# Kernel optimization log

Measured on AMD Instinct MI355X. Metric: run time of the kernel, lower is better.

The kernel has to match this reference:

```python
import jax, jax.numpy as jnp
import numpy as np

B, N, C = 8, 1024, 1024
H = 16
D = C // H  # head_dim = 64
SCALE = D ** -0.5


def setup_inputs() -> dict:
    key = jax.random.key(0)
    k1, k2, k3, k4 = jax.random.split(key, 4)
    x = jax.random.normal(k1, (B, N, C), dtype=jnp.float32)
    qkv_w = jax.random.normal(k2, (3 * C, C), dtype=jnp.float32) * (C ** -0.5)
    proj_w = jax.random.normal(k3, (C, C), dtype=jnp.float32) * (C ** -0.5)
    proj_b = jax.random.normal(k4, (C,), dtype=jnp.float32)
    return {"x": x, "qkv_w": qkv_w, "proj_w": proj_w, "proj_b": proj_b}


def reference(x, qkv_w, proj_w, proj_b):
    # qkv projection: torch Linear weight is [out, in] -> x @ W^T
    qkv = jnp.einsum('bnc,oc->bno', x, qkv_w)            # [B, N, 3C]
    qkv = qkv.reshape(B, N, 3, H, D)
    q = jnp.transpose(qkv[:, :, 0], (0, 2, 1, 3))        # [B, H, N, D]
    k = jnp.transpose(qkv[:, :, 1], (0, 2, 1, 3))
    v = jnp.transpose(qkv[:, :, 2], (0, 2, 1, 3))
    attn = jnp.einsum('bhqd,bhkd->bhqk', q, k) * SCALE   # [B, H, N, N]
    attn = jax.nn.softmax(attn, axis=-1)
    out = jnp.einsum('bhqk,bhkd->bhqd', attn, v)         # [B, H, N, D]
    out = jnp.transpose(out, (0, 2, 1, 3)).reshape(B, N, C)
    out = jnp.einsum('bnc,oc->bno', out, proj_w) + proj_b
    return out
```

## Files before the change

kernel.cpp:

```cpp
#include <hip/hip_runtime.h>
#include <hip/hip_bf16.h>
#include <stdint.h>

#define B_ 8
#define N_ 1024
#define C_ 1024
#define H_ 16

static constexpr float SCALE = 0.125f;
static constexpr float LOG2E = 1.4426950408889634f;
static constexpr float SL    = SCALE * LOG2E;

typedef __attribute__((ext_vector_type(4))) float f32x4;
typedef __attribute__((ext_vector_type(8))) short s16x8;

__device__ __forceinline__ ushort f2bf(float f) {
    union { float f; uint32_t u; } c; c.f = f;
    uint32_t u = c.u;
    return (ushort)((u + 0x7fffu + ((u >> 16) & 1u)) >> 16);
}

__device__ __forceinline__ ushort f2bfc(float f) {
    union { __hip_bfloat16 h; ushort u; } c;
    c.h = __float2bfloat16(f);
    return c.u;
}

__device__ __forceinline__ void gload_lds16(const void* g, void* l) {
    __builtin_amdgcn_global_load_lds(
        (const __attribute__((address_space(1))) void*)g,
        (__attribute__((address_space(3))) void*)l,
        16, 0, 0);
}
__device__ __forceinline__ void gload_lds4(const void* g, void* l) {
    __builtin_amdgcn_global_load_lds(
        (const __attribute__((address_space(1))) void*)g,
        (__attribute__((address_space(3))) void*)l,
        4, 0, 0);
}

__global__ __launch_bounds__(256) void cvt_all(const float* __restrict__ x,
                                               const float* __restrict__ qkv_w,
                                               const float* __restrict__ proj_w,
                                               ushort* __restrict__ xb,
                                               ushort* __restrict__ wqkv,
                                               ushort* __restrict__ wproj) {
    int i = blockIdx.x * 256 + threadIdx.x;
    const float* src;
    ushort* dst;
    float sc = 1.0f;
    if (i < 2097152) {
        src = x; dst = xb;
    } else if (i < 2097152 + 786432) {
        i -= 2097152;
        src = qkv_w; dst = wqkv;
        if (i < 262144) sc = SL;
    } else {
        i -= 2097152 + 786432;
        src = proj_w; dst = wproj;
    }
    float4 v = ((const float4*)src)[i];
    ushort4 o = make_ushort4(f2bf(v.x * sc), f2bf(v.y * sc), f2bf(v.z * sc), f2bf(v.w * sc));
    ((ushort4*)dst)[i] = o;
}

template<int OUT_BF16>
__global__ __launch_bounds__(256) void gemm_bt(const ushort* __restrict__ A,
                                               const ushort* __restrict__ Bw,
                                               void* __restrict__ Cout,
                                               const float* __restrict__ bias,
                                               int M, int Nout, int K) {
    __shared__ ushort Asm[128 * 64];
    __shared__ ushort Bsm[128 * 64];
    const int t = threadIdx.x;
    const int l = t & 63, w = t >> 6;
    const int lq = l & 15, lg = l >> 4;
    const int trow = blockIdx.y * 128, tcol = blockIdx.x * 128;
    const int wrow = (w >> 1) * 64, wcol = (w & 1) * 64;

    f32x4 acc[4][4] = {};

    const int srow0 = t >> 3;
    const int sc8 = (((t & 7) ^ (srow0 & 7)) * 8);
    const size_t abase = (size_t)(trow + srow0) * K + sc8;
    const size_t bbase = (size_t)(tcol + srow0) * K + sc8;

    for (int k0 = 0; k0 < K; k0 += 64) {
#pragma unroll
        for (int i = 0; i < 4; ++i) {
            gload_lds16(A + abase + (size_t)i * 32 * K + k0, &Asm[(i * 256 + w * 64) * 8]);
            gload_lds16(Bw + bbase + (size_t)i * 32 * K + k0, &Bsm[(i * 256 + w * 64) * 8]);
        }
        __syncthreads();
#pragma unroll
        for (int kk = 0; kk < 2; ++kk) {
            s16x8 af[4], bf[4];
#pragma unroll
            for (int m = 0; m < 4; ++m) {
                int row = wrow + m * 16 + lq;
                int ch = (kk * 4 + lg) ^ (row & 7);
                af[m] = *(const s16x8*)&Asm[row * 64 + ch * 8];
            }
#pragma unroll
            for (int n = 0; n < 4; ++n) {
                int row = wcol + n * 16 + lq;
                int ch = (kk * 4 + lg) ^ (row & 7);
                bf[n] = *(const s16x8*)&Bsm[row * 64 + ch * 8];
            }
#pragma unroll
            for (int m = 0; m < 4; ++m)
#pragma unroll
                for (int n = 0; n < 4; ++n)
                    acc[m][n] = __builtin_amdgcn_mfma_f32_16x16x32_bf16(af[m], bf[n], acc[m][n], 0, 0, 0);
        }
        __syncthreads();
    }

#pragma unroll
    for (int m = 0; m < 4; ++m)
#pragma unroll
        for (int n = 0; n < 4; ++n)
#pragma unroll
            for (int r = 0; r < 4; ++r) {
                int row = trow + wrow + m * 16 + lg * 4 + r;
                int col = tcol + wcol + n * 16 + lq;
                if (OUT_BF16) {
                    ((ushort*)Cout)[(size_t)row * Nout + col] = f2bfc(acc[m][n][r]);
                } else {
                    ((float*)Cout)[(size_t)row * Nout + col] = acc[m][n][r] + bias[col];
                }
            }
}

__global__ __launch_bounds__(512, 2) void gemm_bt256(const ushort* __restrict__ A,
                                                     const ushort* __restrict__ Bw,
                                                     ushort* __restrict__ Cout,
                                                     int M, int Nout, int K) {
    __shared__ ushort Asm[2][256 * 64];
    __shared__ ushort Bsm[2][256 * 64];
    const int t = threadIdx.x;
    const int l = t & 63, w = t >> 6;
    const int lq = l & 15, lg = l >> 4;
    const int wm = w >> 2, wn = w & 3;

    int bid = blockIdx.y * gridDim.x + blockIdx.x;
    const int cpx = (gridDim.x * gridDim.y) >> 3;
    bid = (bid & 7) * cpx + (bid >> 3);
    const int bx = bid % gridDim.x, by = bid / gridDim.x;
    const int trow = by * 256, tcol = bx * 256;

    f32x4 acc[8][4] = {};

    const int srow = t >> 3;
    const int scc = ((t & 7) ^ (srow & 7)) * 8;
    const size_t abase = (size_t)(trow + srow) * K + scc;
    const size_t bbase = (size_t)(tcol + srow) * K + scc;

#define STAGE256(buf, k0)                                                      \
    {                                                                          \
        _Pragma("unroll")                                                      \
        for (int j = 0; j < 4; ++j) {                                          \
            gload_lds16(A + abase + (size_t)j * 64 * K + (k0),                 \
                        &Asm[buf][(j * 512 + t) * 8]);                         \
            gload_lds16(Bw + bbase + (size_t)j * 64 * K + (k0),                \
                        &Bsm[buf][(j * 512 + t) * 8]);                         \
        }                                                                      \
    }
#define LOAD_A256(qr)                                                          \
    _Pragma("unroll") for (int m = 0; m < 4; ++m) {                            \
        const int row = wm * 128 + (qr) * 64 + m * 16 + lq;                    \
        _Pragma("unroll") for (int kk = 0; kk < 2; ++kk)                       \
            af[m][kk] = *(const s16x8*)&Asm[cur][row * 64 +                    \
                            (((kk * 4 + lg) ^ (row & 7)) * 8)];                \
    }
#define LOAD_B256(qc)                                                          \
    _Pragma("unroll") for (int n = 0; n < 2; ++n) {                            \
        const int row = wn * 64 + (qc) * 32 + n * 16 + lq;                     \
        _Pragma("unroll") for (int kk = 0; kk < 2; ++kk)                       \
            bf[n][kk] = *(const s16x8*)&Bsm[cur][row * 64 +                    \
                            (((kk * 4 + lg) ^ (row & 7)) * 8)];                \
    }
#define MFMA_Q256(qr, qc)                                                      \
    __builtin_amdgcn_s_setprio(1);                                             \
    _Pragma("unroll") for (int m = 0; m < 4; ++m)                              \
        _Pragma("unroll") for (int n = 0; n < 2; ++n)                          \
            _Pragma("unroll") for (int kk = 0; kk < 2; ++kk)                   \
                acc[(qr) * 4 + m][(qc) * 2 + n] =                              \
                    __builtin_amdgcn_mfma_f32_16x16x32_bf16(                   \
                        af[m][kk], bf[n][kk], acc[(qr) * 4 + m][(qc) * 2 + n], \
                        0, 0, 0);                                              \
    __builtin_amdgcn_s_setprio(0);

    STAGE256(0, 0);
    asm volatile("s_waitcnt vmcnt(0)" ::: "memory");
    __builtin_amdgcn_s_barrier();

    const int NT = K / 64;
    for (int kt = 0; kt < NT; ++kt) {
        const int cur = kt & 1, nxt = cur ^ 1;
        s16x8 af[4][2], bf[2][2];
        LOAD_A256(0); LOAD_B256(0);
        if (kt < NT - 1) STAGE256(nxt, (kt + 1) * 64);
        __builtin_amdgcn_s_barrier();
        MFMA_Q256(0, 0);
        __builtin_amdgcn_s_barrier();
        LOAD_B256(1);
        __builtin_amdgcn_s_barrier();
        MFMA_Q256(0, 1);
        __builtin_amdgcn_s_barrier();
        LOAD_A256(1);
        __builtin_amdgcn_s_barrier();
        MFMA_Q256(1, 1);
        __builtin_amdgcn_s_barrier();
        LOAD_B256(0);
        __builtin_amdgcn_s_barrier();
        MFMA_Q256(1, 0);
        asm volatile("s_waitcnt vmcnt(0)" ::: "memory");
        __builtin_amdgcn_s_barrier();
    }

#pragma unroll
    for (int mt = 0; mt < 8; ++mt)
#pragma unroll
        for (int nt = 0; nt < 4; ++nt)
#pragma unroll
            for (int r = 0; r < 4; ++r) {
                int row = trow + wm * 128 + mt * 16 + lg * 4 + r;
                int col = tcol + wn * 64 + nt * 16 + lq;
                Cout[(size_t)row * Nout + col] = f2bfc(acc[mt][nt][r]);
            }
#undef STAGE256
#undef LOAD_A256
#undef LOAD_B256
#undef MFMA_Q256
}

__global__ __launch_bounds__(512, 4) void attn_fwd(const ushort* __restrict__ qk,
                                                   const ushort* __restrict__ vt,
                                                   ushort* __restrict__ attn_out) {
    __shared__ ushort Klds[64 * 64];
    __shared__ ushort Vlds[64 * 64];

    const int t = threadIdx.x, l = t & 63, w = t >> 6;
    const int lq = l & 15, lg = l >> 4;

    const int serial = blockIdx.x + 4 * blockIdx.y;
    const int logical = (serial & 7) * 64 + (serial >> 3);
    const int qt = logical & 3;
    const int bh = logical >> 2;
    const int b = bh >> 4, h = bh & 15;

    const int qbase = qt * 256 + w * 32 + lq;
    const size_t qoff0 = (size_t)(b * N_ + qbase) * 2048 + h * 64;
    const size_t qoff1 = qoff0 + (size_t)16 * 2048;
    const s16x8 qa0 = *(const s16x8*)&qk[qoff0 + lg * 8];
    const s16x8 qa1 = *(const s16x8*)&qk[qoff0 + 32 + lg * 8];
    const s16x8 qb0 = *(const s16x8*)&qk[qoff1 + lg * 8];
    const s16x8 qb1 = *(const s16x8*)&qk[qoff1 + 32 + lg * 8];

    float lr0 = 0.f, lr1 = 0.f;
    f32x4 o0[4] = {}, o1[4] = {};

    const int srow0 = t >> 3;
    const int sc8 = ((t & 7) ^ (srow0 & 7)) * 8;
    const size_t kgbase = (size_t)(b * N_ + srow0) * 2048 + 1024 + h * 64 + sc8;

    const ushort* vptr[4];
#pragma unroll
    for (int j = 0; j < 4; ++j) {
        const int d = 8 * w + 2 * j + (l >> 5);
        const int c = ((l & 31) >> 2) ^ (d & 7);
        const int s = c * 8 + (l & 3) * 2;
        const int key = (s >> 5) * 32 + ((s >> 2) & 1) * 16 + ((s >> 3) & 3) * 4 + (s & 3);
        vptr[j] = vt + (size_t)(h * 64 + d) * (B_ * N_) + b * N_ + key;
    }

    for (int kt = 0; kt < N_ / 64; ++kt) {
        gload_lds16(qk + kgbase + (size_t)kt * 64 * 2048, &Klds[w * 512]);
#pragma unroll
        for (int j = 0; j < 4; ++j)
            gload_lds4(vptr[j] + kt * 64, &Vlds[w * 512 + j * 128]);
        __syncthreads();

        f32x4 s0[4], s1[4];
#pragma unroll
        for (int g = 0; g < 4; ++g) {
            int key = g * 16 + lq;
            const s16x8 kf0 = *(const s16x8*)&Klds[key * 64 + ((lg ^ (key & 7)) * 8)];
            const s16x8 kf1 = *(const s16x8*)&Klds[key * 64 + (((4 + lg) ^ (key & 7)) * 8)];
            f32x4 z0 = {}, z1 = {};
            z0    = __builtin_amdgcn_mfma_f32_16x16x32_bf16(kf0, qa0, z0, 0, 0, 0);
            s0[g] = __builtin_amdgcn_mfma_f32_16x16x32_bf16(kf1, qa1, z0, 0, 0, 0);
            z1    = __builtin_amdgcn_mfma_f32_16x16x32_bf16(kf0, qb0, z1, 0, 0, 0);
            s1[g] = __builtin_amdgcn_mfma_f32_16x16x32_bf16(kf1, qb1, z1, 0, 0, 0);
        }

#pragma unroll
        for (int kb = 0; kb < 2; ++kb) {
            s16x8 pf0, pf1;
#pragma unroll
            for (int i = 0; i < 4; ++i) {
                float a0 = __builtin_amdgcn_exp2f(s0[2 * kb][i]);
                float a1 = __builtin_amdgcn_exp2f(s0[2 * kb + 1][i]);
                float b0 = __builtin_amdgcn_exp2f(s1[2 * kb][i]);
                float b1 = __builtin_amdgcn_exp2f(s1[2 * kb + 1][i]);
                lr0 += a0 + a1;
                lr1 += b0 + b1;
                pf0[i] = (short)f2bfc(a0); pf0[4 + i] = (short)f2bfc(a1);
                pf1[i] = (short)f2bfc(b0); pf1[4 + i] = (short)f2bfc(b1);
            }
#pragma unroll
            for (int ds = 0; ds < 4; ++ds) {
                const s16x8 vf = *(const s16x8*)
                    &Vlds[(ds * 16 + lq) * 64 + (((kb * 4 + lg) ^ (lq & 7)) * 8)];
                o0[ds] = __builtin_amdgcn_mfma_f32_16x16x32_bf16(pf0, vf, o0[ds], 0, 0, 0);
                o1[ds] = __builtin_amdgcn_mfma_f32_16x16x32_bf16(pf1, vf, o1[ds], 0, 0, 0);
            }
        }
        __syncthreads();
    }

    lr0 += __shfl_xor(lr0, 16); lr0 += __shfl_xor(lr0, 32);
    lr1 += __shfl_xor(lr1, 16); lr1 += __shfl_xor(lr1, 32);

#pragma unroll
    for (int r = 0; r < 4; ++r) {
        float rl0 = 1.f / __shfl(lr0, lg * 4 + r);
        float rl1 = 1.f / __shfl(lr1, lg * 4 + r);
        int orow = qt * 256 + w * 32 + lg * 4 + r;
        size_t base0 = (size_t)(b * N_ + orow) * C_ + h * 64 + lq;
        size_t base1 = base0 + (size_t)16 * C_;
#pragma unroll
        for (int ds = 0; ds < 4; ++ds) {
            attn_out[base0 + ds * 16] = f2bfc(o0[ds][r] * rl0);
            attn_out[base1 + ds * 16] = f2bfc(o1[ds][r] * rl1);
        }
    }
}

extern "C" void kernel_launch(void* const* d_in, const int* in_sizes, int n_in,
                              void* d_out, int out_size, void* d_ws, size_t ws_size,
                              hipStream_t stream) {
    const float* x      = (const float*)d_in[0];
    const float* qkv_w  = (const float*)d_in[1];
    const float* proj_w = (const float*)d_in[2];
    const float* proj_b = (const float*)d_in[3];
    float* out = (float*)d_out;

    ushort* ws    = (ushort*)d_ws;
    ushort* xb    = ws;
    ushort* wqkv  = xb + (size_t)8192 * 1024;
    ushort* wproj = wqkv + (size_t)3072 * 1024;
    ushort* qkb   = wproj + (size_t)1024 * 1024;
    ushort* vtb   = qkb + (size_t)8192 * 2048;
    ushort* attn  = vtb + (size_t)1024 * 8192;

    cvt_all<<<12288, 256, 0, stream>>>(x, qkv_w, proj_w, xb, wqkv, wproj);

    gemm_bt256<<<dim3(8, 32), 512, 0, stream>>>(xb, wqkv, qkb, 8192, 2048, 1024);
    gemm_bt<1><<<dim3(64, 8), 256, 0, stream>>>(wqkv + (size_t)2048 * 1024, xb, (void*)vtb,
                                                nullptr, 1024, 8192, 1024);

    attn_fwd<<<dim3(4, 128), 512, 0, stream>>>(qkb, vtb, attn);

    gemm_bt<0><<<dim3(8, 64), 256, 0, stream>>>(attn, wproj, (void*)out, proj_b, 8192, 1024, 1024);
}
```

Baseline: 145.1 us.

## Widen attention key tile to 128 and drop the 256-tile QK GEMM

The attention kernel now processes 128 keys per iteration instead of 64. K and V LDS buffers are doubled and the V gather pointers and swizzle are remapped for the wider tile, halving the number of barrier-separated iterations. The specialised 256x256 QK projection GEMM is removed and replaced with the generic gemm_bt kernel on a larger grid. The wider tile raises LDS and register use, which may lower occupancy for the 4-blocks-per-CU attention kernel. The generic GEMM may be slower than the tuned 256 tile for the largest GEMM.

```diff
diff --git a/kernel.cpp b/kernel.cpp
--- a/kernel.cpp
+++ b/kernel.cpp
@@ -132,114 +132,11 @@
             }
 }
 
-__global__ __launch_bounds__(512, 2) void gemm_bt256(const ushort* __restrict__ A,
-                                                     const ushort* __restrict__ Bw,
-                                                     ushort* __restrict__ Cout,
-                                                     int M, int Nout, int K) {
-    __shared__ ushort Asm[2][256 * 64];
-    __shared__ ushort Bsm[2][256 * 64];
-    const int t = threadIdx.x;
-    const int l = t & 63, w = t >> 6;
-    const int lq = l & 15, lg = l >> 4;
-    const int wm = w >> 2, wn = w & 3;
-
-    int bid = blockIdx.y * gridDim.x + blockIdx.x;
-    const int cpx = (gridDim.x * gridDim.y) >> 3;
-    bid = (bid & 7) * cpx + (bid >> 3);
-    const int bx = bid % gridDim.x, by = bid / gridDim.x;
-    const int trow = by * 256, tcol = bx * 256;
-
-    f32x4 acc[8][4] = {};
-
-    const int srow = t >> 3;
-    const int scc = ((t & 7) ^ (srow & 7)) * 8;
-    const size_t abase = (size_t)(trow + srow) * K + scc;
-    const size_t bbase = (size_t)(tcol + srow) * K + scc;
-
-#define STAGE256(buf, k0)                                                      \
-    {                                                                          \
-        _Pragma("unroll")                                                      \
-        for (int j = 0; j < 4; ++j) {                                          \
-            gload_lds16(A + abase + (size_t)j * 64 * K + (k0),                 \
-                        &Asm[buf][(j * 512 + t) * 8]);                         \
-            gload_lds16(Bw + bbase + (size_t)j * 64 * K + (k0),                \
-                        &Bsm[buf][(j * 512 + t) * 8]);                         \
-        }                                                                      \
-    }
-#define LOAD_A256(qr)                                                          \
-    _Pragma("unroll") for (int m = 0; m < 4; ++m) {                            \
-        const int row = wm * 128 + (qr) * 64 + m * 16 + lq;                    \
-        _Pragma("unroll") for (int kk = 0; kk < 2; ++kk)                       \
-            af[m][kk] = *(const s16x8*)&Asm[cur][row * 64 +                    \
-                            (((kk * 4 + lg) ^ (row & 7)) * 8)];                \
-    }
-#define LOAD_B256(qc)                                                          \
-    _Pragma("unroll") for (int n = 0; n < 2; ++n) {                            \
-        const int row = wn * 64 + (qc) * 32 + n * 16 + lq;                     \
-        _Pragma("unroll") for (int kk = 0; kk < 2; ++kk)                       \
-            bf[n][kk] = *(const s16x8*)&Bsm[cur][row * 64 +                    \
-                            (((kk * 4 + lg) ^ (row & 7)) * 8)];                \
-    }
-#define MFMA_Q256(qr, qc)                                                      \
-    __builtin_amdgcn_s_setprio(1);                                             \
-    _Pragma("unroll") for (int m = 0; m < 4; ++m)                              \
-        _Pragma("unroll") for (int n = 0; n < 2; ++n)                          \
-            _Pragma("unroll") for (int kk = 0; kk < 2; ++kk)                   \
-                acc[(qr) * 4 + m][(qc) * 2 + n] =                              \
-                    __builtin_amdgcn_mfma_f32_16x16x32_bf16(                   \
-                        af[m][kk], bf[n][kk], acc[(qr) * 4 + m][(qc) * 2 + n], \
-                        0, 0, 0);                                              \
-    __builtin_amdgcn_s_setprio(0);
-
-    STAGE256(0, 0);
-    asm volatile("s_waitcnt vmcnt(0)" ::: "memory");
-    __builtin_amdgcn_s_barrier();
-
-    const int NT = K / 64;
-    for (int kt = 0; kt < NT; ++kt) {
-        const int cur = kt & 1, nxt = cur ^ 1;
-        s16x8 af[4][2], bf[2][2];
-        LOAD_A256(0); LOAD_B256(0);
-        if (kt < NT - 1) STAGE256(nxt, (kt + 1) * 64);
-        __builtin_amdgcn_s_barrier();
-        MFMA_Q256(0, 0);
-        __builtin_amdgcn_s_barrier();
-        LOAD_B256(1);
-        __builtin_amdgcn_s_barrier();
-        MFMA_Q256(0, 1);
-        __builtin_amdgcn_s_barrier();
-        LOAD_A256(1);
-        __builtin_amdgcn_s_barrier();
-        MFMA_Q256(1, 1);
-        __builtin_amdgcn_s_barrier();
-        LOAD_B256(0);
-        __builtin_amdgcn_s_barrier();
-        MFMA_Q256(1, 0);
-        asm volatile("s_waitcnt vmcnt(0)" ::: "memory");
-        __builtin_amdgcn_s_barrier();
-    }
-
-#pragma unroll
-    for (int mt = 0; mt < 8; ++mt)
-#pragma unroll
-        for (int nt = 0; nt < 4; ++nt)
-#pragma unroll
-            for (int r = 0; r < 4; ++r) {
-                int row = trow + wm * 128 + mt * 16 + lg * 4 + r;
-                int col = tcol + wn * 64 + nt * 16 + lq;
-                Cout[(size_t)row * Nout + col] = f2bfc(acc[mt][nt][r]);
-            }
-#undef STAGE256
-#undef LOAD_A256
-#undef LOAD_B256
-#undef MFMA_Q256
-}
-
 __global__ __launch_bounds__(512, 4) void attn_fwd(const ushort* __restrict__ qk,
                                                    const ushort* __restrict__ vt,
                                                    ushort* __restrict__ attn_out) {
-    __shared__ ushort Klds[64 * 64];
-    __shared__ ushort Vlds[64 * 64];
+    __shared__ ushort Klds[128 * 64];
+    __shared__ ushort Vlds[64 * 128];
 
     const int t = threadIdx.x, l = t & 63, w = t >> 6;
     const int lq = l & 15, lg = l >> 4;
@@ -265,26 +162,28 @@
     const int sc8 = ((t & 7) ^ (srow0 & 7)) * 8;
     const size_t kgbase = (size_t)(b * N_ + srow0) * 2048 + 1024 + h * 64 + sc8;
 
-    const ushort* vptr[4];
-#pragma unroll
-    for (int j = 0; j < 4; ++j) {
-        const int d = 8 * w + 2 * j + (l >> 5);
-        const int c = ((l & 31) >> 2) ^ (d & 7);
+    const ushort* vptr[8];
+#pragma unroll
+    for (int j = 0; j < 8; ++j) {
+        const int d = w * 8 + j;
+        const int c = (l >> 2) ^ (d & 7);
         const int s = c * 8 + (l & 3) * 2;
-        const int key = (s >> 5) * 32 + ((s >> 2) & 1) * 16 + ((s >> 3) & 3) * 4 + (s & 3);
+        const int key = (2 * (s >> 5) + ((s >> 2) & 1)) * 16 + ((s >> 3) & 3) * 4 + (s & 3);
         vptr[j] = vt + (size_t)(h * 64 + d) * (B_ * N_) + b * N_ + key;
     }
 
-    for (int kt = 0; kt < N_ / 64; ++kt) {
-        gload_lds16(qk + kgbase + (size_t)kt * 64 * 2048, &Klds[w * 512]);
-#pragma unroll
-        for (int j = 0; j < 4; ++j)
-            gload_lds4(vptr[j] + kt * 64, &Vlds[w * 512 + j * 128]);
-        __syncthreads();
-
-        f32x4 s0[4], s1[4];
-#pragma unroll
-        for (int g = 0; g < 4; ++g) {
+    for (int kt = 0; kt < N_ / 128; ++kt) {
+        const size_t koff = kgbase + (size_t)kt * 128 * 2048;
+        gload_lds16(qk + koff, &Klds[w * 512]);
+        gload_lds16(qk + koff + (size_t)64 * 2048, &Klds[4096 + w * 512]);
+#pragma unroll
+        for (int j = 0; j < 8; ++j)
+            gload_lds4(vptr[j] + kt * 128, &Vlds[(w * 8 + j) * 128]);
+        __syncthreads();
+
+        f32x4 s0[8], s1[8];
+#pragma unroll
+        for (int g = 0; g < 8; ++g) {
             int key = g * 16 + lq;
             const s16x8 kf0 = *(const s16x8*)&Klds[key * 64 + ((lg ^ (key & 7)) * 8)];
             const s16x8 kf1 = *(const s16x8*)&Klds[key * 64 + (((4 + lg) ^ (key & 7)) * 8)];
@@ -296,7 +195,7 @@
         }
 
 #pragma unroll
-        for (int kb = 0; kb < 2; ++kb) {
+        for (int kb = 0; kb < 4; ++kb) {
             s16x8 pf0, pf1;
 #pragma unroll
             for (int i = 0; i < 4; ++i) {
@@ -312,7 +211,7 @@
 #pragma unroll
             for (int ds = 0; ds < 4; ++ds) {
                 const s16x8 vf = *(const s16x8*)
-                    &Vlds[(ds * 16 + lq) * 64 + (((kb * 4 + lg) ^ (lq & 7)) * 8)];
+                    &Vlds[(ds * 16 + lq) * 128 + (((kb * 4 + lg) ^ (lq & 7)) * 8)];
                 o0[ds] = __builtin_amdgcn_mfma_f32_16x16x32_bf16(pf0, vf, o0[ds], 0, 0, 0);
                 o1[ds] = __builtin_amdgcn_mfma_f32_16x16x32_bf16(pf1, vf, o1[ds], 0, 0, 0);
             }
@@ -357,7 +256,7 @@
 
     cvt_all<<<12288, 256, 0, stream>>>(x, qkv_w, proj_w, xb, wqkv, wproj);
 
-    gemm_bt256<<<dim3(8, 32), 512, 0, stream>>>(xb, wqkv, qkb, 8192, 2048, 1024);
+    gemm_bt<1><<<dim3(16, 64), 256, 0, stream>>>(xb, wqkv, (void*)qkb, nullptr, 8192, 2048, 1024);
     gemm_bt<1><<<dim3(64, 8), 256, 0, stream>>>(wqkv + (size_t)2048 * 1024, xb, (void*)vtb,
                                                 nullptr, 1024, 8192, 1024);
 
```

Measured after the change: 197.5 us. 36.1% more time.
